# Kernel optimization log

Measured on AMD Instinct MI355X. Metric: run time of the kernel, lower is better.

Reference implementation:

```python
import jax, jax.numpy as jnp
import numpy as np

KSIZE = 5
DILATION = 1
DYN = 32  # dynamic (value) channels


def setup_inputs() -> dict:
    key = jax.random.key(0)
    k1, k2 = jax.random.split(key)
    x = jax.random.normal(k1, (4, 64, 256, 256), dtype=jnp.float32)
    kernel = jax.random.normal(k2, (KSIZE * KSIZE, 1), dtype=jnp.float32)
    return {"input": x, "kernel": kernel}


def _neighborhoods(x):
    """Gather KxK dilated neighborhoods with zero padding.
    x: [B, C, H, W] -> [B, C, K^2, H, W], taps in row-major (i, j) order
    matching nn.Unfold."""
    B, C, H, W = x.shape
    pad = DILATION * (KSIZE // 2)
    xp = jnp.pad(x, ((0, 0), (0, 0), (pad, pad), (pad, pad)))
    taps = [xp[:, :, i * DILATION:i * DILATION + H, j * DILATION:j * DILATION + W]
            for i in range(KSIZE) for j in range(KSIZE)]
    return jnp.stack(taps, axis=2)


def reference(input, kernel):
    x = input
    nbrs = _neighborhoods(x)                      # [B, C, K2, H, W]
    # scores over static channels (c >= DYN) against center pixel, scaled by
    # learned per-tap kernel weight / kernel_size
    scores = jnp.einsum('bckhw,bchw->bkhw', nbrs[:, DYN:], x[:, DYN:])
    scores = scores * (kernel[:, 0][None, :, None, None] / KSIZE)
    smax = jax.nn.softmax(scores, axis=1)          # softmax over K^2 taps
    # weighted sum of dynamic channels
    out = jnp.einsum('bkhw,bckhw->bchw', smax, nbrs[:, :DYN])
    return out
```

## Files before the change

kernel.cpp:

```cpp
#include <hip/hip_runtime.h>
#include <math.h>

#define KS    5
#define K2    25
#define BB    4
#define HH    256
#define WW    256
#define PLANE (HH * WW)
#define LROWD 264
#define PTILE 1864
#define NTHR  256

typedef __attribute__((ext_vector_type(2))) _Float16 half2_t;
typedef __attribute__((ext_vector_type(4))) float    f32x4;

static __device__ __forceinline__ half2_t u2h(unsigned u) { return __builtin_bit_cast(half2_t, u); }

static __device__ __forceinline__ unsigned pkrtz(float a, float b) {
    auto h = __builtin_amdgcn_cvt_pkrtz(a, b);
    return __builtin_bit_cast(unsigned, h);
}

static __device__ __forceinline__ float dot2(half2_t a, half2_t b, float c) {
#if __has_builtin(__builtin_amdgcn_fdot2)
    return __builtin_amdgcn_fdot2(a, b, c, false);
#else
    return (float)a.x * (float)b.x + ((float)a.y * (float)b.y + c);
#endif
}

__global__ __launch_bounds__(NTHR, 2)
void local_attn_kernel(const float* __restrict__ x,
                       const float* __restrict__ kern,
                       float* __restrict__ out)
{
    __shared__ unsigned ldsu[2 * 4 * PTILE];
    __shared__ float kw[K2];

    const int tid = threadIdx.x;
    for (int i = tid; i < 2 * 4 * PTILE; i += NTHR) ldsu[i] = 0u;
    if (tid < K2) kw[tid] = kern[tid] * (1.0f / KS);

    const int lane = tid & 63;
    const int wv   = tid >> 6;
    const int ty   = wv >> 1;
    const int cg   = lane >> 5;
    const int tx   = ((wv & 1) << 5) | (lane & 31);
    const int w0   = tx << 2;

    const int bx     = blockIdx.x;
    const int hgroup = ((bx & 7) << 4) | (bx >> 3);
    const int h0     = hgroup * 2;
    const int h      = h0 + ty;
    const int b      = blockIdx.y;

    const float* xb = x + (size_t)b * 64 * PLANE;

    int gofs[6], lofs[6], pofs[6];
#pragma unroll
    for (int i = 0; i < 6; ++i) {
        const int rp   = (tid >> 6) + 4 * i;
        const int row  = rp % 6;
        const int pair = rp / 6;
        const int r    = h0 - 2 + row;
        const bool v   = (unsigned)r < (unsigned)HH;
        gofs[i] = min(max(r, 0), HH - 1) * WW + (tid & 63) * 4;
        pofs[i] = pair * 2 * PLANE;
        lofs[i] = pair * PTILE + (v ? row : 6) * LROWD + 2 + (tid & 63) * 4;
    }

    f32x4 pa[6], pb[6];
    auto prefetch = [&](int st) {
        const float* xc = xb + (size_t)((st < 4) ? 32 + st * 8 : (st - 4) * 8) * PLANE;
#pragma unroll
        for (int i = 0; i < 6; ++i) {
            const float* p0 = xc + pofs[i] + gofs[i];
            const float* p1 = p0 + PLANE;
            asm volatile("global_load_dwordx4 %0, %1, off"
                         : "=v"(pa[i]) : "v"(p0));
            asm volatile("global_load_dwordx4 %0, %1, off"
                         : "=v"(pb[i]) : "v"(p1));
        }
        __builtin_amdgcn_sched_barrier(0);
    };
    auto cvtwrite = [&](int bufi) {
        asm volatile("s_waitcnt vmcnt(0)" ::: "memory");
        __builtin_amdgcn_sched_barrier(0);
        unsigned* lb = ldsu + bufi * 4 * PTILE;
#pragma unroll
        for (int i = 0; i < 6; ++i) {
            const unsigned d0 = pkrtz(pa[i].x, pb[i].x);
            const unsigned d1 = pkrtz(pa[i].y, pb[i].y);
            const unsigned d2 = pkrtz(pa[i].z, pb[i].z);
            const unsigned d3 = pkrtz(pa[i].w, pb[i].w);
            *(uint2*)(lb + lofs[i])     = make_uint2(d0, d1);
            *(uint2*)(lb + lofs[i] + 2) = make_uint2(d2, d3);
        }
    };

    float s[4][K2];
#pragma unroll
    for (int p = 0; p < 4; ++p)
#pragma unroll
        for (int k = 0; k < K2; ++k) s[p][k] = 0.0f;

    __syncthreads();
    prefetch(0);
    cvtwrite(0);
    __syncthreads();

#pragma unroll 1
    for (int t = 0; t < 8; ++t) {
        if (t + 1 < 8) prefetch(t + 1);
        const unsigned* buf = ldsu + (t & 1) * 4 * PTILE;

        if (t < 4) {
#pragma unroll
            for (int dp = 0; dp < 2; ++dp) {
                const unsigned* tb = buf + (cg * 2 + dp) * PTILE;
                half2_t ctr[4];
                {
                    const unsigned* rp = tb + (ty + 2) * LROWD + w0;
                    const uint4 r0 = *(const uint4*)(rp);
                    const uint4 r1 = *(const uint4*)(rp + 4);
                    half2_t f[8] = {u2h(r0.x), u2h(r0.y), u2h(r0.z), u2h(r0.w),
                                    u2h(r1.x), u2h(r1.y), u2h(r1.z), u2h(r1.w)};
#pragma unroll
                    for (int p = 0; p < 4; ++p) ctr[p] = f[p + 2];
#pragma unroll
                    for (int j = 0; j < KS; ++j)
#pragma unroll
                        for (int p = 0; p < 4; ++p)
                            s[p][2 * KS + j] = dot2(f[p + j], ctr[p], s[p][2 * KS + j]);
                }
#pragma unroll
                for (int i = 0; i < KS; ++i) {
                    if (i == 2) continue;
                    const unsigned* rp = tb + (ty + i) * LROWD + w0;
                    const uint4 r0 = *(const uint4*)(rp);
                    const uint4 r1 = *(const uint4*)(rp + 4);
                    half2_t f[8] = {u2h(r0.x), u2h(r0.y), u2h(r0.z), u2h(r0.w),
                                    u2h(r1.x), u2h(r1.y), u2h(r1.z), u2h(r1.w)};
#pragma unroll
                    for (int j = 0; j < KS; ++j)
#pragma unroll
                        for (int p = 0; p < 4; ++p)
                            s[p][i * KS + j] = dot2(f[p + j], ctr[p], s[p][i * KS + j]);
                }
            }
            if (t == 3) {
#pragma unroll
                for (int p = 0; p < 4; ++p)
#pragma unroll
                    for (int k = 0; k < K2; ++k)
                        s[p][k] += __shfl_xor(s[p][k], 32, 64);
#pragma unroll
                for (int p = 0; p < 4; ++p) {
                    float mx = -INFINITY;
#pragma unroll
                    for (int k = 0; k < K2; ++k) {
                        float v = s[p][k] * kw[k];
                        s[p][k] = v;
                        mx = fmaxf(mx, v);
                    }
                    float sum = 0.0f;
#pragma unroll
                    for (int k = 0; k < K2; ++k) {
                        float e = __expf(s[p][k] - mx);
                        s[p][k] = e;
                        sum += e;
                    }
                    const float inv = 1.0f / sum;
#pragma unroll
                    for (int k = 0; k < K2; ++k) s[p][k] *= inv;
                }
            }
        } else {
            const int chb = (t - 4) * 8;
#pragma unroll
            for (int dp = 0; dp < 2; ++dp) {
                const unsigned* tb = buf + (cg * 2 + dp) * PTILE;
                float alo[4] = {0.f, 0.f, 0.f, 0.f};
                float ahi[4] = {0.f, 0.f, 0.f, 0.f};
#pragma unroll
                for (int i = 0; i < KS; ++i) {
                    const unsigned* rp = tb + (ty + i) * LROWD + w0;
                    const uint4 r0 = *(const uint4*)(rp);
                    const uint4 r1 = *(const uint4*)(rp + 4);
                    half2_t f[8] = {u2h(r0.x), u2h(r0.y), u2h(r0.z), u2h(r0.w),
                                    u2h(r1.x), u2h(r1.y), u2h(r1.z), u2h(r1.w)};
#pragma unroll
                    for (int j = 0; j < KS; ++j)
#pragma unroll
                        for (int p = 0; p < 4; ++p) {
                            const half2_t v = f[p + j];
                            const float  wgt = s[p][i * KS + j];
                            alo[p] = fmaf((float)v.x, wgt, alo[p]);
                            ahi[p] = fmaf((float)v.y, wgt, ahi[p]);
                        }
                }
                const int c0 = chb + (cg * 2 + dp) * 2;
                float* op = out + ((size_t)b * 32 + c0) * PLANE + h * WW + w0;
                *(float4*)op           = make_float4(alo[0], alo[1], alo[2], alo[3]);
                *(float4*)(op + PLANE) = make_float4(ahi[0], ahi[1], ahi[2], ahi[3]);
            }
        }

        if (t + 1 < 8) {
            cvtwrite((t + 1) & 1);
            __syncthreads();
        }
    }
}

extern "C" void kernel_launch(void* const* d_in, const int* in_sizes, int n_in,
                              void* d_out, int out_size, void* d_ws, size_t ws_size,
                              hipStream_t stream) {
    const float* x    = (const float*)d_in[0];
    const float* kern = (const float*)d_in[1];
    float*       out  = (float*)d_out;

    dim3 grid(HH / 2, BB, 1);
    dim3 block(NTHR, 1, 1);
    hipLaunchKernelGGL(local_attn_kernel, grid, block, 0, stream, x, kern, out);
}
```

Before: 107.6 us.

## Split row tiles into half-width column tiles with 128-thread blocks

Each block now covers a 128-column half of two output rows instead of the full width, so the grid doubles and blocks shrink to 128 threads. Halo columns are loaded as clamped 4-wide segments, with edge-shift selection and a dump slot for out-of-range writes. The aim is more, smaller blocks with less LDS each, giving better occupancy and balance across CUs. The cost is redundant halo loads at tile edges, more complex per-segment addressing, and an occupancy hint pinned to 2 waves per EU.

```diff
diff --git a/kernel.cpp b/kernel.cpp
--- a/kernel.cpp
+++ b/kernel.cpp
@@ -7,9 +7,14 @@
 #define HH    256
 #define WW    256
 #define PLANE (HH * WW)
-#define LROWD 264
-#define PTILE 1864
-#define NTHR  256
+#define TW    128
+#define LROWD 136
+#define PTILE 820
+#define BSTR  (4 * PTILE + LROWD)
+#define DUMPO (4 * PTILE)
+#define NTHR  128
+#define NSEG  816
+#define SPT   7
 
 typedef __attribute__((ext_vector_type(2))) _Float16 half2_t;
 typedef __attribute__((ext_vector_type(4))) float    f32x4;
@@ -29,51 +34,67 @@
 #endif
 }
 
-__global__ __launch_bounds__(NTHR, 2)
+__global__ __launch_bounds__(NTHR, 4) __attribute__((amdgpu_waves_per_eu(2, 2)))
 void local_attn_kernel(const float* __restrict__ x,
                        const float* __restrict__ kern,
                        float* __restrict__ out)
 {
-    __shared__ unsigned ldsu[2 * 4 * PTILE];
+    __shared__ unsigned ldsu[2 * BSTR];
     __shared__ float kw[K2];
 
     const int tid = threadIdx.x;
-    for (int i = tid; i < 2 * 4 * PTILE; i += NTHR) ldsu[i] = 0u;
+    for (int i = tid; i < 2 * BSTR; i += NTHR) ldsu[i] = 0u;
     if (tid < K2) kw[tid] = kern[tid] * (1.0f / KS);
 
     const int lane = tid & 63;
-    const int wv   = tid >> 6;
-    const int ty   = wv >> 1;
+    const int ty   = tid >> 6;
     const int cg   = lane >> 5;
-    const int tx   = ((wv & 1) << 5) | (lane & 31);
-    const int w0   = tx << 2;
+    const int txg  = lane & 31;
+    const int w0   = txg << 2;
 
     const int bx     = blockIdx.x;
-    const int hgroup = ((bx & 7) << 4) | (bx >> 3);
+    const int wseg   = bx & 1;
+    const int bxh    = bx >> 1;
+    const int hgroup = ((bxh & 7) << 4) | (bxh >> 3);
     const int h0     = hgroup * 2;
     const int h      = h0 + ty;
+    const int wbase  = wseg * TW;
     const int b      = blockIdx.y;
 
     const float* xb = x + (size_t)b * 64 * PLANE;
 
-    int gofs[6], lofs[6], pofs[6];
-#pragma unroll
-    for (int i = 0; i < 6; ++i) {
-        const int rp   = (tid >> 6) + 4 * i;
-        const int row  = rp % 6;
-        const int pair = rp / 6;
+    int gofs[SPT], pofs[SPT], lofsA[SPT], lofsB[SPT];
+    bool lsh[SPT], rsh[SPT];
+#pragma unroll
+    for (int i = 0; i < SPT; ++i) {
+        const int seg0 = tid + i * NTHR;
+        const bool segv = seg0 < NSEG;
+        const int seg  = segv ? seg0 : NSEG - 1;
+        const int pair = seg / 204;
+        const int rem  = seg - pair * 204;
+        const int row  = rem / 34;
+        const int sg   = rem - row * 34;
         const int r    = h0 - 2 + row;
-        const bool v   = (unsigned)r < (unsigned)HH;
-        gofs[i] = min(max(r, 0), HH - 1) * WW + (tid & 63) * 4;
+        const bool rv  = (unsigned)r < (unsigned)HH;
+        const int c0   = wbase - 2 + sg * 4;
+        const int cl   = min(max(c0, 0), WW - 4);
+        gofs[i] = min(max(r, 0), HH - 1) * WW + cl;
         pofs[i] = pair * 2 * PLANE;
-        lofs[i] = pair * PTILE + (v ? row : 6) * LROWD + 2 + (tid & 63) * 4;
+        const int db = row * LROWD + sg * 4;
+        const bool Av = segv && rv && (sg < 33) && (c0 >= 0) && (c0 + 1 < WW);
+        const bool Bv = segv && rv && (sg < 33) && (c0 + 3 < WW);
+        lsh[i] = (c0 == -2);
+        rsh[i] = (c0 == WW - 2);
+        const int dump = DUMPO + (tid & 31) * 4;
+        lofsA[i] = Av ? pair * PTILE + db     : dump;
+        lofsB[i] = Bv ? pair * PTILE + db + 2 : dump + 2;
     }
 
-    f32x4 pa[6], pb[6];
+    f32x4 pa[SPT], pb[SPT];
     auto prefetch = [&](int st) {
         const float* xc = xb + (size_t)((st < 4) ? 32 + st * 8 : (st - 4) * 8) * PLANE;
 #pragma unroll
-        for (int i = 0; i < 6; ++i) {
+        for (int i = 0; i < SPT; ++i) {
             const float* p0 = xc + pofs[i] + gofs[i];
             const float* p1 = p0 + PLANE;
             asm volatile("global_load_dwordx4 %0, %1, off"
@@ -86,15 +107,17 @@
     auto cvtwrite = [&](int bufi) {
         asm volatile("s_waitcnt vmcnt(0)" ::: "memory");
         __builtin_amdgcn_sched_barrier(0);
-        unsigned* lb = ldsu + bufi * 4 * PTILE;
-#pragma unroll
-        for (int i = 0; i < 6; ++i) {
+        unsigned* lb = ldsu + bufi * BSTR;
+#pragma unroll
+        for (int i = 0; i < SPT; ++i) {
             const unsigned d0 = pkrtz(pa[i].x, pb[i].x);
             const unsigned d1 = pkrtz(pa[i].y, pb[i].y);
             const unsigned d2 = pkrtz(pa[i].z, pb[i].z);
             const unsigned d3 = pkrtz(pa[i].w, pb[i].w);
-            *(uint2*)(lb + lofs[i])     = make_uint2(d0, d1);
-            *(uint2*)(lb + lofs[i] + 2) = make_uint2(d2, d3);
+            const uint2 sA = rsh[i] ? make_uint2(d2, d3) : make_uint2(d0, d1);
+            const uint2 sB = lsh[i] ? make_uint2(d0, d1) : make_uint2(d2, d3);
+            *(uint2*)(lb + lofsA[i]) = sA;
+            *(uint2*)(lb + lofsB[i]) = sB;
         }
     };
 
@@ -112,7 +135,7 @@
 #pragma unroll 1
     for (int t = 0; t < 8; ++t) {
         if (t + 1 < 8) prefetch(t + 1);
-        const unsigned* buf = ldsu + (t & 1) * 4 * PTILE;
+        const unsigned* buf = ldsu + (t & 1) * BSTR;
 
         if (t < 4) {
 #pragma unroll
@@ -200,7 +223,7 @@
                         }
                 }
                 const int c0 = chb + (cg * 2 + dp) * 2;
-                float* op = out + ((size_t)b * 32 + c0) * PLANE + h * WW + w0;
+                float* op = out + ((size_t)b * 32 + c0) * PLANE + h * WW + wbase + w0;
                 *(float4*)op           = make_float4(alo[0], alo[1], alo[2], alo[3]);
                 *(float4*)(op + PLANE) = make_float4(ahi[0], ahi[1], ahi[2], ahi[3]);
             }
@@ -220,7 +243,7 @@
     const float* kern = (const float*)d_in[1];
     float*       out  = (float*)d_out;
 
-    dim3 grid(HH / 2, BB, 1);
+    dim3 grid(2 * (HH / 2), BB, 1);
     dim3 block(NTHR, 1, 1);
     hipLaunchKernelGGL(local_attn_kernel, grid, block, 0, stream, x, kern, out);
 }
```

New measurement: 120.8 us. 12.3% more time.

## Add dedicated producer wavefront for global loads into LDS double buffer

Applied to the files above, without the earlier changes.

Adds a fifth wavefront per block that alone issues the global loads, converts them to fp16 and writes them into the LDS double buffer, pipelining channel pairs with partial vmcnt waits. The four compute wavefronts no longer prefetch and only consume LDS, syncing with the producer once per stage. This is meant to separate memory latency from the compute waves and free their registers. In exchange, a single wave now issues all loads, which may limit memory-level parallelism, and block size grows to 320 threads, which can affect occupancy.

```diff
diff --git a/kernel.cpp b/kernel.cpp
--- a/kernel.cpp
+++ b/kernel.cpp
@@ -9,7 +9,7 @@
 #define PLANE (HH * WW)
 #define LROWD 264
 #define PTILE 1864
-#define NTHR  256
+#define NTHR  320
 
 typedef __attribute__((ext_vector_type(2))) _Float16 half2_t;
 typedef __attribute__((ext_vector_type(4))) float    f32x4;
@@ -43,171 +43,186 @@
 
     const int lane = tid & 63;
     const int wv   = tid >> 6;
-    const int ty   = wv >> 1;
-    const int cg   = lane >> 5;
-    const int tx   = ((wv & 1) << 5) | (lane & 31);
-    const int w0   = tx << 2;
 
     const int bx     = blockIdx.x;
     const int hgroup = ((bx & 7) << 4) | (bx >> 3);
     const int h0     = hgroup * 2;
-    const int h      = h0 + ty;
     const int b      = blockIdx.y;
 
     const float* xb = x + (size_t)b * 64 * PLANE;
 
-    int gofs[6], lofs[6], pofs[6];
-#pragma unroll
-    for (int i = 0; i < 6; ++i) {
-        const int rp   = (tid >> 6) + 4 * i;
-        const int row  = rp % 6;
-        const int pair = rp / 6;
-        const int r    = h0 - 2 + row;
-        const bool v   = (unsigned)r < (unsigned)HH;
-        gofs[i] = min(max(r, 0), HH - 1) * WW + (tid & 63) * 4;
-        pofs[i] = pair * 2 * PLANE;
-        lofs[i] = pair * PTILE + (v ? row : 6) * LROWD + 2 + (tid & 63) * 4;
-    }
-
-    f32x4 pa[6], pb[6];
-    auto prefetch = [&](int st) {
-        const float* xc = xb + (size_t)((st < 4) ? 32 + st * 8 : (st - 4) * 8) * PLANE;
-#pragma unroll
-        for (int i = 0; i < 6; ++i) {
-            const float* p0 = xc + pofs[i] + gofs[i];
-            const float* p1 = p0 + PLANE;
-            asm volatile("global_load_dwordx4 %0, %1, off"
-                         : "=v"(pa[i]) : "v"(p0));
-            asm volatile("global_load_dwordx4 %0, %1, off"
-                         : "=v"(pb[i]) : "v"(p1));
+    __syncthreads();
+
+    if (wv == 4) {
+        int grow[6], lrow[6];
+#pragma unroll
+        for (int rr = 0; rr < 6; ++rr) {
+            const int r  = h0 - 2 + rr;
+            const bool v = (unsigned)r < (unsigned)HH;
+            grow[rr] = min(max(r, 0), HH - 1) * WW + lane * 4;
+            lrow[rr] = (v ? rr : 6) * LROWD + 2 + lane * 4;
         }
-        __builtin_amdgcn_sched_barrier(0);
-    };
-    auto cvtwrite = [&](int bufi) {
-        asm volatile("s_waitcnt vmcnt(0)" ::: "memory");
-        __builtin_amdgcn_sched_barrier(0);
-        unsigned* lb = ldsu + bufi * 4 * PTILE;
-#pragma unroll
-        for (int i = 0; i < 6; ++i) {
-            const unsigned d0 = pkrtz(pa[i].x, pb[i].x);
-            const unsigned d1 = pkrtz(pa[i].y, pb[i].y);
-            const unsigned d2 = pkrtz(pa[i].z, pb[i].z);
-            const unsigned d3 = pkrtz(pa[i].w, pb[i].w);
-            *(uint2*)(lb + lofs[i])     = make_uint2(d0, d1);
-            *(uint2*)(lb + lofs[i] + 2) = make_uint2(d2, d3);
+
+        f32x4 A0[6], B0[6], A1[6], B1[6];
+
+        auto issue = [&](const float* xc, int pair, f32x4* A, f32x4* B) {
+#pragma unroll
+            for (int rr = 0; rr < 6; ++rr) {
+                const float* p0 = xc + pair * 2 * PLANE + grow[rr];
+                const float* p1 = p0 + PLANE;
+                asm volatile("global_load_dwordx4 %0, %1, off" : "=v"(A[rr]) : "v"(p0));
+                asm volatile("global_load_dwordx4 %0, %1, off" : "=v"(B[rr]) : "v"(p1));
+            }
+        };
+        auto cvtw = [&](unsigned* lb, int pair, const f32x4* A, const f32x4* B) {
+#pragma unroll
+            for (int rr = 0; rr < 6; ++rr) {
+                unsigned* wp = lb + pair * PTILE + lrow[rr];
+                const unsigned d0 = pkrtz(A[rr].x, B[rr].x);
+                const unsigned d1 = pkrtz(A[rr].y, B[rr].y);
+                const unsigned d2 = pkrtz(A[rr].z, B[rr].z);
+                const unsigned d3 = pkrtz(A[rr].w, B[rr].w);
+                *(uint2*)(wp)     = make_uint2(d0, d1);
+                *(uint2*)(wp + 2) = make_uint2(d2, d3);
+            }
+        };
+        auto stage = [&](int st) {
+            const float* xc = xb + (size_t)((st < 4) ? 32 + st * 8 : (st - 4) * 8) * PLANE;
+            unsigned* lb = ldsu + (st & 1) * 4 * PTILE;
+            issue(xc, 0, A0, B0);
+            issue(xc, 1, A1, B1);
+            asm volatile("s_waitcnt vmcnt(12)" ::: "memory");
+            __builtin_amdgcn_sched_barrier(0);
+            cvtw(lb, 0, A0, B0);
+            issue(xc, 2, A0, B0);
+            asm volatile("s_waitcnt vmcnt(12)" ::: "memory");
+            __builtin_amdgcn_sched_barrier(0);
+            cvtw(lb, 1, A1, B1);
+            issue(xc, 3, A1, B1);
+            asm volatile("s_waitcnt vmcnt(12)" ::: "memory");
+            __builtin_amdgcn_sched_barrier(0);
+            cvtw(lb, 2, A0, B0);
+            asm volatile("s_waitcnt vmcnt(0)" ::: "memory");
+            __builtin_amdgcn_sched_barrier(0);
+            cvtw(lb, 3, A1, B1);
+        };
+
+        stage(0);
+        __syncthreads();
+#pragma unroll 1
+        for (int t = 0; t < 8; ++t) {
+            if (t < 7) stage(t + 1);
+            __syncthreads();
         }
-    };
-
-    float s[4][K2];
-#pragma unroll
-    for (int p = 0; p < 4; ++p)
-#pragma unroll
-        for (int k = 0; k < K2; ++k) s[p][k] = 0.0f;
-
-    __syncthreads();
-    prefetch(0);
-    cvtwrite(0);
-    __syncthreads();
-
+    } else {
+        const int ty = wv >> 1;
+        const int cg = lane >> 5;
+        const int tx = ((wv & 1) << 5) | (lane & 31);
+        const int w0 = tx << 2;
+        const int h  = h0 + ty;
+
+        float s[4][K2];
+#pragma unroll
+        for (int p = 0; p < 4; ++p)
+#pragma unroll
+            for (int k = 0; k < K2; ++k) s[p][k] = 0.0f;
+
+        __syncthreads();
 #pragma unroll 1
-    for (int t = 0; t < 8; ++t) {
-        if (t + 1 < 8) prefetch(t + 1);
-        const unsigned* buf = ldsu + (t & 1) * 4 * PTILE;
-
-        if (t < 4) {
-#pragma unroll
-            for (int dp = 0; dp < 2; ++dp) {
-                const unsigned* tb = buf + (cg * 2 + dp) * PTILE;
-                half2_t ctr[4];
-                {
-                    const unsigned* rp = tb + (ty + 2) * LROWD + w0;
-                    const uint4 r0 = *(const uint4*)(rp);
-                    const uint4 r1 = *(const uint4*)(rp + 4);
-                    half2_t f[8] = {u2h(r0.x), u2h(r0.y), u2h(r0.z), u2h(r0.w),
-                                    u2h(r1.x), u2h(r1.y), u2h(r1.z), u2h(r1.w)};
-#pragma unroll
-                    for (int p = 0; p < 4; ++p) ctr[p] = f[p + 2];
-#pragma unroll
-                    for (int j = 0; j < KS; ++j)
-#pragma unroll
-                        for (int p = 0; p < 4; ++p)
-                            s[p][2 * KS + j] = dot2(f[p + j], ctr[p], s[p][2 * KS + j]);
+        for (int t = 0; t < 8; ++t) {
+            const unsigned* buf = ldsu + (t & 1) * 4 * PTILE;
+
+            if (t < 4) {
+#pragma unroll
+                for (int dp = 0; dp < 2; ++dp) {
+                    const unsigned* tb = buf + (cg * 2 + dp) * PTILE;
+                    half2_t ctr[4];
+                    {
+                        const unsigned* rp = tb + (ty + 2) * LROWD + w0;
+                        const uint4 r0 = *(const uint4*)(rp);
+                        const uint4 r1 = *(const uint4*)(rp + 4);
+                        half2_t f[8] = {u2h(r0.x), u2h(r0.y), u2h(r0.z), u2h(r0.w),
+                                        u2h(r1.x), u2h(r1.y), u2h(r1.z), u2h(r1.w)};
+#pragma unroll
+                        for (int p = 0; p < 4; ++p) ctr[p] = f[p + 2];
+#pragma unroll
+                        for (int j = 0; j < KS; ++j)
+#pragma unroll
+                            for (int p = 0; p < 4; ++p)
+                                s[p][2 * KS + j] = dot2(f[p + j], ctr[p], s[p][2 * KS + j]);
+                    }
+#pragma unroll
+                    for (int i = 0; i < KS; ++i) {
+                        if (i == 2) continue;
+                        const unsigned* rp = tb + (ty + i) * LROWD + w0;
+                        const uint4 r0 = *(const uint4*)(rp);
+                        const uint4 r1 = *(const uint4*)(rp + 4);
+                        half2_t f[8] = {u2h(r0.x), u2h(r0.y), u2h(r0.z), u2h(r0.w),
+                                        u2h(r1.x), u2h(r1.y), u2h(r1.z), u2h(r1.w)};
+#pragma unroll
+                        for (int j = 0; j < KS; ++j)
+#pragma unroll
+                            for (int p = 0; p < 4; ++p)
+                                s[p][i * KS + j] = dot2(f[p + j], ctr[p], s[p][i * KS + j]);
+                    }
                 }
-#pragma unroll
-                for (int i = 0; i < KS; ++i) {
-                    if (i == 2) continue;
-                    const unsigned* rp = tb + (ty + i) * LROWD + w0;
-                    const uint4 r0 = *(const uint4*)(rp);
-                    const uint4 r1 = *(const uint4*)(rp + 4);
-                    half2_t f[8] = {u2h(r0.x), u2h(r0.y), u2h(r0.z), u2h(r0.w),
-                                    u2h(r1.x), u2h(r1.y), u2h(r1.z), u2h(r1.w)};
-#pragma unroll
-                    for (int j = 0; j < KS; ++j)
-#pragma unroll
-                        for (int p = 0; p < 4; ++p)
-                            s[p][i * KS + j] = dot2(f[p + j], ctr[p], s[p][i * KS + j]);
+                if (t == 3) {
+#pragma unroll
+                    for (int p = 0; p < 4; ++p)
+#pragma unroll
+                        for (int k = 0; k < K2; ++k)
+                            s[p][k] += __shfl_xor(s[p][k], 32, 64);
+#pragma unroll
+                    for (int p = 0; p < 4; ++p) {
+                        float mx = -INFINITY;
+#pragma unroll
+                        for (int k = 0; k < K2; ++k) {
+                            float v = s[p][k] * kw[k];
+                            s[p][k] = v;
+                            mx = fmaxf(mx, v);
+                        }
+                        float sum = 0.0f;
+#pragma unroll
+                        for (int k = 0; k < K2; ++k) {
+                            float e = __expf(s[p][k] - mx);
+                            s[p][k] = e;
+                            sum += e;
+                        }
+                        const float inv = 1.0f / sum;
+#pragma unroll
+                        for (int k = 0; k < K2; ++k) s[p][k] *= inv;
+                    }
+                }
+            } else {
+                const int chb = (t - 4) * 8;
+#pragma unroll
+                for (int dp = 0; dp < 2; ++dp) {
+                    const unsigned* tb = buf + (cg * 2 + dp) * PTILE;
+                    float alo[4] = {0.f, 0.f, 0.f, 0.f};
+                    float ahi[4] = {0.f, 0.f, 0.f, 0.f};
+#pragma unroll
+                    for (int i = 0; i < KS; ++i) {
+                        const unsigned* rp = tb + (ty + i) * LROWD + w0;
+                        const uint4 r0 = *(const uint4*)(rp);
+                        const uint4 r1 = *(const uint4*)(rp + 4);
+                        half2_t f[8] = {u2h(r0.x), u2h(r0.y), u2h(r0.z), u2h(r0.w),
+                                        u2h(r1.x), u2h(r1.y), u2h(r1.z), u2h(r1.w)};
+#pragma unroll
+                        for (int j = 0; j < KS; ++j)
+#pragma unroll
+                            for (int p = 0; p < 4; ++p) {
+                                const half2_t v = f[p + j];
+                                const float  wgt = s[p][i * KS + j];
+                                alo[p] = fmaf((float)v.x, wgt, alo[p]);
+                                ahi[p] = fmaf((float)v.y, wgt, ahi[p]);
+                            }
+                    }
+                    const int c0 = chb + (cg * 2 + dp) * 2;
+                    float* op = out + ((size_t)b * 32 + c0) * PLANE + h * WW + w0;
+                    *(float4*)op           = make_float4(alo[0], alo[1], alo[2], alo[3]);
+                    *(float4*)(op + PLANE) = make_float4(ahi[0], ahi[1], ahi[2], ahi[3]);
                 }
             }
-            if (t == 3) {
-#pragma unroll
-                for (int p = 0; p < 4; ++p)
-#pragma unroll
-                    for (int k = 0; k < K2; ++k)
-                        s[p][k] += __shfl_xor(s[p][k], 32, 64);
-#pragma unroll
-                for (int p = 0; p < 4; ++p) {
-                    float mx = -INFINITY;
-#pragma unroll
-                    for (int k = 0; k < K2; ++k) {
-                        float v = s[p][k] * kw[k];
-                        s[p][k] = v;
-                        mx = fmaxf(mx, v);
-                    }
-                    float sum = 0.0f;
-#pragma unroll
-                    for (int k = 0; k < K2; ++k) {
-                        float e = __expf(s[p][k] - mx);
-                        s[p][k] = e;
-                        sum += e;
-                    }
-                    const float inv = 1.0f / sum;
-#pragma unroll
-                    for (int k = 0; k < K2; ++k) s[p][k] *= inv;
-                }
-            }
-        } else {
-            const int chb = (t - 4) * 8;
-#pragma unroll
-            for (int dp = 0; dp < 2; ++dp) {
-                const unsigned* tb = buf + (cg * 2 + dp) * PTILE;
-                float alo[4] = {0.f, 0.f, 0.f, 0.f};
-                float ahi[4] = {0.f, 0.f, 0.f, 0.f};
-#pragma unroll
-                for (int i = 0; i < KS; ++i) {
-                    const unsigned* rp = tb + (ty + i) * LROWD + w0;
-                    const uint4 r0 = *(const uint4*)(rp);
-                    const uint4 r1 = *(const uint4*)(rp + 4);
-                    half2_t f[8] = {u2h(r0.x), u2h(r0.y), u2h(r0.z), u2h(r0.w),
-                                    u2h(r1.x), u2h(r1.y), u2h(r1.z), u2h(r1.w)};
-#pragma unroll
-                    for (int j = 0; j < KS; ++j)
-#pragma unroll
-                        for (int p = 0; p < 4; ++p) {
-                            const half2_t v = f[p + j];
-                            const float  wgt = s[p][i * KS + j];
-                            alo[p] = fmaf((float)v.x, wgt, alo[p]);
-                            ahi[p] = fmaf((float)v.y, wgt, ahi[p]);
-                        }
-                }
-                const int c0 = chb + (cg * 2 + dp) * 2;
-                float* op = out + ((size_t)b * 32 + c0) * PLANE + h * WW + w0;
-                *(float4*)op           = make_float4(alo[0], alo[1], alo[2], alo[3]);
-                *(float4*)(op + PLANE) = make_float4(ahi[0], ahi[1], ahi[2], ahi[3]);
-            }
-        }
-
-        if (t + 1 < 8) {
-            cvtwrite((t + 1) & 1);
             __syncthreads();
         }
     }
```

Measured after the change: 116.6 us. +8.4%, slower.

## Split softmax taps across half-waves to cut score register footprint

Applied to the files above, without the earlier changes.

Instead of splitting channel pairs across the two half-waves, each half-wave now handles all channel pairs but only about half of the 25 taps, holding 13 scores per pixel instead of 25. The two halves swap partial scores with a cross-lane shuffle for the softmax, and reduce partial outputs with shuffles before one half writes. The aim is lower VGPR pressure (paired with an explicit waves-per-EU attribute), traded for more LDS row reads per channel pair, added shuffles and select instructions, and half the lanes idle on stores.

```diff
diff --git a/kernel.cpp b/kernel.cpp
--- a/kernel.cpp
+++ b/kernel.cpp
@@ -29,7 +29,7 @@
 #endif
 }
 
-__global__ __launch_bounds__(NTHR, 2)
+__global__ __launch_bounds__(NTHR, 2) __attribute__((amdgpu_waves_per_eu(2)))
 void local_attn_kernel(const float* __restrict__ x,
                        const float* __restrict__ kern,
                        float* __restrict__ out)
@@ -45,6 +45,7 @@
     const int wv   = tid >> 6;
     const int ty   = wv >> 1;
     const int cg   = lane >> 5;
+    const bool hi  = (cg != 0);
     const int tx   = ((wv & 1) << 5) | (lane & 31);
     const int w0   = tx << 2;
 
@@ -98,11 +99,11 @@
         }
     };
 
-    float s[4][K2];
+    float s[4][13];
 #pragma unroll
     for (int p = 0; p < 4; ++p)
 #pragma unroll
-        for (int k = 0; k < K2; ++k) s[p][k] = 0.0f;
+        for (int m = 0; m < 13; ++m) s[p][m] = 0.0f;
 
     __syncthreads();
     prefetch(0);
@@ -116,93 +117,141 @@
 
         if (t < 4) {
 #pragma unroll
-            for (int dp = 0; dp < 2; ++dp) {
-                const unsigned* tb = buf + (cg * 2 + dp) * PTILE;
+            for (int dp = 0; dp < 4; ++dp) {
+                const unsigned* tb = buf + dp * PTILE;
+                const unsigned* rA = tb + (ty + (hi ? 3 : 0)) * LROWD + w0;
+                const unsigned* rC = tb + (ty + 2) * LROWD + w0;
+                const uint4 A0 = *(const uint4*)(rA);
+                const uint4 A1 = *(const uint4*)(rA + 4);
+                const uint4 B0 = *(const uint4*)(rA + LROWD);
+                const uint4 B1 = *(const uint4*)(rA + LROWD + 4);
+                const uint4 C0 = *(const uint4*)(rC);
+                const uint4 C1 = *(const uint4*)(rC + 4);
+                const unsigned fa[8] = {A0.x, A0.y, A0.z, A0.w, A1.x, A1.y, A1.z, A1.w};
+                const unsigned fb[8] = {B0.x, B0.y, B0.z, B0.w, B1.x, B1.y, B1.z, B1.w};
+                const unsigned fc[8] = {C0.x, C0.y, C0.z, C0.w, C1.x, C1.y, C1.z, C1.w};
                 half2_t ctr[4];
-                {
-                    const unsigned* rp = tb + (ty + 2) * LROWD + w0;
-                    const uint4 r0 = *(const uint4*)(rp);
-                    const uint4 r1 = *(const uint4*)(rp + 4);
-                    half2_t f[8] = {u2h(r0.x), u2h(r0.y), u2h(r0.z), u2h(r0.w),
-                                    u2h(r1.x), u2h(r1.y), u2h(r1.z), u2h(r1.w)};
-#pragma unroll
-                    for (int p = 0; p < 4; ++p) ctr[p] = f[p + 2];
-#pragma unroll
-                    for (int j = 0; j < KS; ++j)
-#pragma unroll
-                        for (int p = 0; p < 4; ++p)
-                            s[p][2 * KS + j] = dot2(f[p + j], ctr[p], s[p][2 * KS + j]);
-                }
-#pragma unroll
-                for (int i = 0; i < KS; ++i) {
-                    if (i == 2) continue;
-                    const unsigned* rp = tb + (ty + i) * LROWD + w0;
-                    const uint4 r0 = *(const uint4*)(rp);
-                    const uint4 r1 = *(const uint4*)(rp + 4);
-                    half2_t f[8] = {u2h(r0.x), u2h(r0.y), u2h(r0.z), u2h(r0.w),
-                                    u2h(r1.x), u2h(r1.y), u2h(r1.z), u2h(r1.w)};
-#pragma unroll
-                    for (int j = 0; j < KS; ++j)
-#pragma unroll
-                        for (int p = 0; p < 4; ++p)
-                            s[p][i * KS + j] = dot2(f[p + j], ctr[p], s[p][i * KS + j]);
-                }
+#pragma unroll
+                for (int p = 0; p < 4; ++p) ctr[p] = u2h(fc[p + 2]);
+                unsigned g[6];
+#pragma unroll
+                for (int q = 0; q < 6; ++q) g[q] = hi ? fc[q + 2] : fc[q];
+#pragma unroll
+                for (int j = 0; j < KS; ++j)
+#pragma unroll
+                    for (int p = 0; p < 4; ++p)
+                        s[p][j] = dot2(u2h(fa[p + j]), ctr[p], s[p][j]);
+#pragma unroll
+                for (int j = 0; j < KS; ++j)
+#pragma unroll
+                    for (int p = 0; p < 4; ++p)
+                        s[p][5 + j] = dot2(u2h(fb[p + j]), ctr[p], s[p][5 + j]);
+#pragma unroll
+                for (int jj = 0; jj < 3; ++jj)
+#pragma unroll
+                    for (int p = 0; p < 4; ++p)
+                        s[p][10 + jj] = dot2(u2h(g[p + jj]), ctr[p], s[p][10 + jj]);
             }
             if (t == 3) {
 #pragma unroll
-                for (int p = 0; p < 4; ++p)
-#pragma unroll
-                    for (int k = 0; k < K2; ++k)
-                        s[p][k] += __shfl_xor(s[p][k], 32, 64);
-#pragma unroll
                 for (int p = 0; p < 4; ++p) {
+                    float r[13];
+#pragma unroll
+                    for (int m = 0; m < 13; ++m) r[m] = __shfl_xor(s[p][m], 32, 64);
+                    float sc[K2];
+#pragma unroll
+                    for (int m = 0; m < 10; ++m) sc[m] = hi ? r[m] : s[p][m];
+                    sc[10] = hi ? r[10] : s[p][10];
+                    sc[11] = hi ? r[11] : s[p][11];
+                    sc[12] = hi ? r[12] : s[p][12];
+                    sc[13] = hi ? s[p][11] : r[11];
+                    sc[14] = hi ? s[p][12] : r[12];
+#pragma unroll
+                    for (int m = 0; m < 10; ++m) sc[15 + m] = hi ? s[p][m] : r[m];
                     float mx = -INFINITY;
 #pragma unroll
                     for (int k = 0; k < K2; ++k) {
-                        float v = s[p][k] * kw[k];
-                        s[p][k] = v;
+                        float v = sc[k] * kw[k];
+                        sc[k] = v;
                         mx = fmaxf(mx, v);
                     }
                     float sum = 0.0f;
 #pragma unroll
                     for (int k = 0; k < K2; ++k) {
-                        float e = __expf(s[p][k] - mx);
-                        s[p][k] = e;
+                        float e = __expf(sc[k] - mx);
+                        sc[k] = e;
                         sum += e;
                     }
                     const float inv = 1.0f / sum;
 #pragma unroll
-                    for (int k = 0; k < K2; ++k) s[p][k] *= inv;
+                    for (int k = 0; k < K2; ++k) sc[k] *= inv;
+#pragma unroll
+                    for (int m = 0; m < 10; ++m) s[p][m] = hi ? sc[15 + m] : sc[m];
+                    s[p][10] = hi ? 0.0f : sc[10];
+                    s[p][11] = hi ? sc[13] : sc[11];
+                    s[p][12] = hi ? sc[14] : sc[12];
                 }
             }
         } else {
             const int chb = (t - 4) * 8;
 #pragma unroll
-            for (int dp = 0; dp < 2; ++dp) {
-                const unsigned* tb = buf + (cg * 2 + dp) * PTILE;
+            for (int dp = 0; dp < 4; ++dp) {
+                const unsigned* tb = buf + dp * PTILE;
+                const unsigned* rA = tb + (ty + (hi ? 3 : 0)) * LROWD + w0;
+                const unsigned* rC = tb + (ty + 2) * LROWD + w0;
+                const uint4 A0 = *(const uint4*)(rA);
+                const uint4 A1 = *(const uint4*)(rA + 4);
+                const uint4 B0 = *(const uint4*)(rA + LROWD);
+                const uint4 B1 = *(const uint4*)(rA + LROWD + 4);
+                const uint4 C0 = *(const uint4*)(rC);
+                const uint4 C1 = *(const uint4*)(rC + 4);
+                const unsigned fa[8] = {A0.x, A0.y, A0.z, A0.w, A1.x, A1.y, A1.z, A1.w};
+                const unsigned fb[8] = {B0.x, B0.y, B0.z, B0.w, B1.x, B1.y, B1.z, B1.w};
+                const unsigned fc[8] = {C0.x, C0.y, C0.z, C0.w, C1.x, C1.y, C1.z, C1.w};
+                unsigned g[6];
+#pragma unroll
+                for (int q = 0; q < 6; ++q) g[q] = hi ? fc[q + 2] : fc[q];
+
                 float alo[4] = {0.f, 0.f, 0.f, 0.f};
                 float ahi[4] = {0.f, 0.f, 0.f, 0.f};
 #pragma unroll
-                for (int i = 0; i < KS; ++i) {
-                    const unsigned* rp = tb + (ty + i) * LROWD + w0;
-                    const uint4 r0 = *(const uint4*)(rp);
-                    const uint4 r1 = *(const uint4*)(rp + 4);
-                    half2_t f[8] = {u2h(r0.x), u2h(r0.y), u2h(r0.z), u2h(r0.w),
-                                    u2h(r1.x), u2h(r1.y), u2h(r1.z), u2h(r1.w)};
-#pragma unroll
-                    for (int j = 0; j < KS; ++j)
-#pragma unroll
-                        for (int p = 0; p < 4; ++p) {
-                            const half2_t v = f[p + j];
-                            const float  wgt = s[p][i * KS + j];
-                            alo[p] = fmaf((float)v.x, wgt, alo[p]);
-                            ahi[p] = fmaf((float)v.y, wgt, ahi[p]);
-                        }
+                for (int j = 0; j < KS; ++j)
+#pragma unroll
+                    for (int p = 0; p < 4; ++p) {
+                        const half2_t v = u2h(fa[p + j]);
+                        const float  w = s[p][j];
+                        alo[p] = fmaf((float)v.x, w, alo[p]);
+                        ahi[p] = fmaf((float)v.y, w, ahi[p]);
+                    }
+#pragma unroll
+                for (int j = 0; j < KS; ++j)
+#pragma unroll
+                    for (int p = 0; p < 4; ++p) {
+                        const half2_t v = u2h(fb[p + j]);
+                        const float  w = s[p][5 + j];
+                        alo[p] = fmaf((float)v.x, w, alo[p]);
+                        ahi[p] = fmaf((float)v.y, w, ahi[p]);
+                    }
+#pragma unroll
+                for (int jj = 0; jj < 3; ++jj)
+#pragma unroll
+                    for (int p = 0; p < 4; ++p) {
+                        const half2_t v = u2h(g[p + jj]);
+                        const float  w = s[p][10 + jj];
+                        alo[p] = fmaf((float)v.x, w, alo[p]);
+                        ahi[p] = fmaf((float)v.y, w, ahi[p]);
+                    }
+#pragma unroll
+                for (int p = 0; p < 4; ++p) {
+                    alo[p] += __shfl_xor(alo[p], 32, 64);
+                    ahi[p] += __shfl_xor(ahi[p], 32, 64);
                 }
-                const int c0 = chb + (cg * 2 + dp) * 2;
-                float* op = out + ((size_t)b * 32 + c0) * PLANE + h * WW + w0;
-                *(float4*)op           = make_float4(alo[0], alo[1], alo[2], alo[3]);
-                *(float4*)(op + PLANE) = make_float4(ahi[0], ahi[1], ahi[2], ahi[3]);
+                const int c0 = chb + dp * 2;
+                if (cg == (dp & 1)) {
+                    float* op = out + ((size_t)b * 32 + c0) * PLANE + h * WW + w0;
+                    *(float4*)op           = make_float4(alo[0], alo[1], alo[2], alo[3]);
+                    *(float4*)(op + PLANE) = make_float4(ahi[0], ahi[1], ahi[2], ahi[3]);
+                }
             }
         }
 
```

Measured after the change: 111.9 us. 4.0% more time.
